# Optimization experiments

Measured on AMD Instinct MI355X. Metric: run time of the kernel, lower is better.

Reference implementation:

```python
import math
import jax, jax.numpy as jnp
import numpy as np

B, T, C = 2, 2048, 1024
H, HKV, HD = 16, 4, 64  # n_head, n_kv_head, head_dim
G = H // HKV            # GQA groups
WS = 1024               # sliding window size
GATE_CH = 32


def setup_inputs() -> dict:
    key = jax.random.key(0)
    ks = jax.random.split(key, 8)
    x = jax.random.normal(ks[0], (B, T, C), dtype=jnp.float32)
    ve = jax.random.normal(ks[1], (B, T, HKV * HD), dtype=jnp.float32)
    # realistic RoPE tables: half head_dim frequencies
    d = HD // 2
    inv_freq = 1.0 / (10000.0 ** (jnp.arange(d, dtype=jnp.float32) / d))
    angles = jnp.arange(T, dtype=jnp.float32)[:, None] * inv_freq[None, :]  # (T, d)
    cos = jnp.cos(angles)[None, :, None, :]  # (1, T, 1, d)
    sin = jnp.sin(angles)[None, :, None, :]
    s = 0.02
    Wq = s * jax.random.normal(ks[2], (C, H * HD), dtype=jnp.float32)
    Wk = s * jax.random.normal(ks[3], (C, HKV * HD), dtype=jnp.float32)
    Wv = s * jax.random.normal(ks[4], (C, HKV * HD), dtype=jnp.float32)
    Wproj = s * jax.random.normal(ks[5], (C, C), dtype=jnp.float32)
    Wg = s * jax.random.normal(ks[6], (GATE_CH, HKV), dtype=jnp.float32)
    return {"x": x, "ve": ve, "cos": cos, "sin": sin,
            "Wq": Wq, "Wk": Wk, "Wv": Wv, "Wproj": Wproj, "Wg": Wg, "ws": WS}


def _rope(u, cos, sin):
    d = u.shape[-1] // 2
    u1, u2 = u[..., :d], u[..., d:]
    return jnp.concatenate([u1 * cos + u2 * sin, -u1 * sin + u2 * cos], axis=-1)


def _rmsnorm(u):
    eps = jnp.finfo(u.dtype).eps
    return u * jax.lax.rsqrt(jnp.mean(u * u, axis=-1, keepdims=True) + eps)


def reference(x, ve, cos, sin, Wq, Wk, Wv, Wproj, Wg, ws):
    b, t, c = x.shape
    q = (x @ Wq).reshape(b, t, H, HD)
    k = (x @ Wk).reshape(b, t, HKV, HD)
    v = (x @ Wv).reshape(b, t, HKV, HD)
    # value-embedding gate: 2*sigmoid over first 32 channels of x
    gate = 2.0 * jax.nn.sigmoid(x[..., :GATE_CH] @ Wg)  # (b, t, HKV)
    v = v + gate[..., None] * ve.reshape(b, t, HKV, HD)
    q = _rmsnorm(_rope(q, cos, sin))
    k = _rmsnorm(_rope(k, cos, sin))
    # GQA: view q as (b, t, HKV, G, HD), contract against shared k/v per kv-head
    qg = q.reshape(b, t, HKV, G, HD)
    scale = 1.0 / math.sqrt(HD)
    scores = jnp.einsum('bqhgd,bkhd->bhgqk', qg, k) * scale  # (b, HKV, G, t, t)
    pos = jnp.arange(t)
    # key j attends iff i - ws + 1 <= j <= i (sliding causal window)
    mask = (pos[None, :] >= pos[:, None] - ws + 1) & (pos[None, :] <= pos[:, None])
    scores = jnp.where(mask[None, None, None], scores, -jnp.inf)
    attn = jax.nn.softmax(scores, axis=-1)
    y = jnp.einsum('bhgqk,bkhd->bqhgd', attn, v).reshape(b, t, H * HD)
    return y @ Wproj
```

## Files before the change

### kernel.cpp

```cpp
#include <hip/hip_runtime.h>
#include <hip/hip_bf16.h>

#define Bq 2
#define Tq 2048
#define Cq 1024
#define Hq 16
#define HKVq 4
#define HDq 64
#define Gq 4
#define WSq 1024
#define GATE_CHq 32

typedef __attribute__((ext_vector_type(8))) short short8;
typedef __attribute__((ext_vector_type(4))) float f32x4;
typedef __attribute__((ext_vector_type(2))) unsigned int u32x2;
typedef unsigned int u32;
typedef unsigned short u16;

#if __has_builtin(__builtin_amdgcn_exp2f)
#define EXP2(x) __builtin_amdgcn_exp2f(x)
#else
#define EXP2(x) exp2f(x)
#endif

__device__ __forceinline__ u16 f2bf(float f) {
  u32 u = __float_as_uint(f);
  u32 r = (u + 0x7FFFu + ((u >> 16) & 1u)) >> 16;
  return (u16)r;
}
__device__ __forceinline__ float bf2f(u16 u) {
  return __uint_as_float(((u32)u) << 16);
}

__device__ __forceinline__ void gl_lds16(const u16* g, u16* l) {
  __builtin_amdgcn_global_load_lds(
      (const u32 __attribute__((address_space(1)))*)g,
      (u32 __attribute__((address_space(3)))*)l, 16, 0, 0);
}

template <bool BF16OUT>
__global__ __launch_bounds__(256) void gemm_bt(
    const u16* __restrict__ A, const u16* __restrict__ Bt,
    void* __restrict__ Cv, int M, int N, int K) {
  __shared__ __attribute__((aligned(16))) u16 As[64 * 32];
  __shared__ __attribute__((aligned(16))) u16 Bs[128 * 32];

  const int bm0 = blockIdx.y * 64, bn0 = blockIdx.x * 128;
  const int tid = threadIdx.x;
  const int w = tid >> 6, lane = tid & 63;
  const int wm = (w >> 1) * 32, wn = (w & 1) * 64;
  const int quad = lane >> 4, l16 = lane & 15;

  f32x4 acc[2][4];
#pragma unroll
  for (int mt = 0; mt < 2; mt++)
#pragma unroll
    for (int nt = 0; nt < 4; nt++) acc[mt][nt] = (f32x4){0.f, 0.f, 0.f, 0.f};

  const int mA = tid >> 2, gpA = tid & 3;
  const int goffA = mA * K + (gpA ^ ((mA >> 1) & 3)) * 8;
  int goffB[2];
#pragma unroll
  for (int i = 0; i < 2; i++) {
    int s = i * 256 + tid;
    int m = s >> 2, gp = s & 3;
    goffB[i] = m * K + (gp ^ ((m >> 1) & 3)) * 8;
  }
  const u16* Ab = A + (long)bm0 * K;
  const u16* Bb = Bt + (long)bn0 * K;

  const u16* pA[2];
  const u16* pB[4];
#pragma unroll
  for (int t = 0; t < 2; t++) {
    int ml = wm + t * 16 + l16;
    pA[t] = &As[(ml * 4 + (quad ^ ((ml >> 1) & 3))) * 8];
  }
#pragma unroll
  for (int t = 0; t < 4; t++) {
    int nl = wn + t * 16 + l16;
    pB[t] = &Bs[(nl * 4 + (quad ^ ((nl >> 1) & 3))) * 8];
  }

  for (int k0 = 0; k0 < K; k0 += 32) {
    __syncthreads();
    gl_lds16(Ab + goffA + k0, &As[(w * 64) * 8]);
#pragma unroll
    for (int i = 0; i < 2; i++)
      gl_lds16(Bb + goffB[i] + k0, &Bs[(i * 256 + w * 64) * 8]);
    __syncthreads();

    short8 af[2], bf[4];
#pragma unroll
    for (int t = 0; t < 2; t++) af[t] = *(const short8*)pA[t];
#pragma unroll
    for (int t = 0; t < 4; t++) bf[t] = *(const short8*)pB[t];
#pragma unroll
    for (int mt = 0; mt < 2; mt++)
#pragma unroll
      for (int nt = 0; nt < 4; nt++)
        acc[mt][nt] = __builtin_amdgcn_mfma_f32_16x16x32_bf16(
            af[mt], bf[nt], acc[mt][nt], 0, 0, 0);
  }

#pragma unroll
  for (int mt = 0; mt < 2; mt++)
#pragma unroll
    for (int nt = 0; nt < 4; nt++) {
      int row0 = bm0 + wm + mt * 16 + quad * 4;
      int col = bn0 + wn + nt * 16 + l16;
#pragma unroll
      for (int r = 0; r < 4; r++) {
        if (BF16OUT)
          ((u16*)Cv)[(long)(row0 + r) * N + col] = f2bf(acc[mt][nt][r]);
        else
          ((float*)Cv)[(long)(row0 + r) * N + col] = acc[mt][nt][r];
      }
    }
}

__global__ __launch_bounds__(256) void cast_bf16(const float* __restrict__ S,
                                                 u16* __restrict__ D) {
  int i = (blockIdx.x * 256 + threadIdx.x) * 8;
  float4 a = *(const float4*)(S + i);
  float4 b = *(const float4*)(S + i + 4);
  union { short8 v; u16 u[8]; } o;
  o.u[0] = f2bf(a.x); o.u[1] = f2bf(a.y); o.u[2] = f2bf(a.z); o.u[3] = f2bf(a.w);
  o.u[4] = f2bf(b.x); o.u[5] = f2bf(b.y); o.u[6] = f2bf(b.z); o.u[7] = f2bf(b.w);
  *(short8*)(D + i) = o.v;
}

__device__ __forceinline__ void wtrans_body(const float* __restrict__ S,
                                            u16* __restrict__ D, int N, int n0,
                                            int k0, float (*tile)[65]) {
  int tid = threadIdx.x;
#pragma unroll
  for (int i = 0; i < 16; i++) {
    int idx = i * 256 + tid;
    int kl = idx >> 6, nl = idx & 63;
    tile[kl][nl] = S[(long)(k0 + kl) * N + n0 + nl];
  }
  __syncthreads();
#pragma unroll
  for (int i = 0; i < 16; i++) {
    int idx = i * 256 + tid;
    int nl = idx >> 6, kl = idx & 63;
    D[(long)(n0 + nl) * 1024 + k0 + kl] = f2bf(tile[kl][nl]);
  }
}

__global__ __launch_bounds__(256) void wtrans(const float* __restrict__ S,
                                              u16* __restrict__ D, int N) {
  __shared__ float tile[64][65];
  wtrans_body(S, D, N, blockIdx.x * 64, blockIdx.y * 64, tile);
}

__global__ __launch_bounds__(256) void wtrans_qkv(
    const float* __restrict__ Wq, const float* __restrict__ Wk,
    const float* __restrict__ Wv, u16* __restrict__ D) {
  __shared__ float tile[64][65];
  int bx = blockIdx.x;
  const float* S;
  u16* Dst;
  int N, nb;
  if (bx < 16)      { S = Wq; N = 1024; nb = bx;      Dst = D; }
  else if (bx < 20) { S = Wk; N = 256;  nb = bx - 16; Dst = D + 1024 * 1024; }
  else              { S = Wv; N = 256;  nb = bx - 20; Dst = D + 1280 * 1024; }
  wtrans_body(S, Dst, N, nb * 64, blockIdx.y * 64, tile);
}

__device__ __forceinline__ float rope_rms(float u, int lane, float c, float s) {
  float up = __shfl_xor(u, 32);
  float r = (lane < 32) ? (u * c + up * s) : (u * c - up * s);
  float sum = r * r;
#pragma unroll
  for (int off = 32; off >= 1; off >>= 1) sum += __shfl_xor(sum, off);
  return r * rsqrtf(sum * (1.f / 64.f) + 1.1920928955078125e-07f);
}

__global__ __launch_bounds__(256) void postproc(
    const float* __restrict__ x, const float* __restrict__ ve,
    const float* __restrict__ cosp, const float* __restrict__ sinp,
    const float* __restrict__ Wg, const u16* __restrict__ QKV,
    u16* __restrict__ Qb, u16* __restrict__ Kb, u16* __restrict__ Vb) {
  int bt = blockIdx.x;
  int b = bt >> 11;
  int t = bt & (Tq - 1);
  int tid = threadIdx.x;
  int w = tid >> 6;
  int lane = tid & 63;
  const u16* row = QKV + (long)bt * 1536;

  float c = cosp[t * 32 + (lane & 31)];
  float s = sinp[t * 32 + (lane & 31)];

  float pg = 0.f;
  if (lane < 32) pg = x[(long)bt * Cq + lane] * Wg[lane * HKVq + w];
#pragma unroll
  for (int off = 16; off >= 1; off >>= 1) pg += __shfl_xor(pg, off);
  float z = __shfl(pg, 0);
  float gate = 2.f / (1.f + expf(-z));

  long vi = (long)bt * (HKVq * HDq) + w * HDq + lane;
  float v = bf2f(row[1280 + w * HDq + lane]) + gate * ve[vi];
  Vb[((long)((b * 4 + w) * Tq + t)) * 64 + lane] = f2bf(v);

  float kv = rope_rms(bf2f(row[1024 + w * HDq + lane]), lane, c, s);
  Kb[((long)((b * 4 + w) * Tq + t)) * 64 + lane] = f2bf(kv);

#pragma unroll
  for (int hi = 0; hi < 4; hi++) {
    int h = hi * 4 + w;
    float q = rope_rms(bf2f(row[h * HDq + lane]), lane, c, s);
    Qb[((long)(((b * 4 + hi) * 4 + w) * Tq + t)) * 64 + lane] = f2bf(q);
  }
}

__global__ __launch_bounds__(256) void vtrans(const u16* __restrict__ Vb,
                                              u16* __restrict__ Vtb) {
  __shared__ u16 tile[64][74];
  int bh = blockIdx.y;
  int t0 = blockIdx.x * 64;
  int tid = threadIdx.x;
  const u16* src = Vb + ((long)bh * Tq + t0) * 64;
  u16* dst = Vtb + (long)bh * 64 * Tq + t0;
#pragma unroll
  for (int i = 0; i < 16; i++) {
    int idx = i * 256 + tid;
    int r = idx >> 6, cl = idx & 63;
    tile[r][cl] = src[(long)r * 64 + cl];
  }
  __syncthreads();
#pragma unroll
  for (int i = 0; i < 16; i++) {
    int idx = i * 256 + tid;
    int d = idx >> 6, t = idx & 63;
    dst[(long)d * Tq + t] = tile[t][d];
  }
}

#define CEXP 0.18033688011112042f
#define CEXP8 1.4426950408889634f

__device__ __forceinline__ void attn_tile(
    int k0, bool maskC, bool maskW, int qpos, int quad, int l16,
    const u16* __restrict__ Ks, const u16* __restrict__ Vts,
    u32* __restrict__ myPs, short8 QB0, short8 QB1, f32x4* O, float& lsum) {
  f32x4 S4[4];
#pragma unroll
  for (int nt = 0; nt < 4; nt++) {
    int key = nt * 16 + l16;
    short8 kb0 = *(const short8*)(&Ks[key * 64 + ((quad ^ (key & 7)) * 8)]);
    short8 kb1 = *(const short8*)(&Ks[key * 64 + (((quad + 4) ^ (key & 7)) * 8)]);
    f32x4 acc = (f32x4){0.f, 0.f, 0.f, 0.f};
    acc = __builtin_amdgcn_mfma_f32_16x16x32_bf16(kb0, QB0, acc, 0, 0, 0);
    acc = __builtin_amdgcn_mfma_f32_16x16x32_bf16(kb1, QB1, acc, 0, 0, 0);
    S4[nt] = acc;
  }

  float Pv[4][4];
#pragma unroll
  for (int nt = 0; nt < 4; nt++) {
#pragma unroll
    for (int r = 0; r < 4; r++) {
      float sv = S4[nt][r];
      if (maskC || maskW) {
        int kpos = k0 + nt * 16 + quad * 4 + r;
        bool valid = true;
        if (maskC) valid = valid && (kpos <= qpos);
        if (maskW) valid = valid && (kpos >= qpos - (WSq - 1));
        sv = valid ? sv : -1e30f;
      }
      float p = EXP2(__builtin_fmaf(sv, CEXP, -CEXP8));
      Pv[nt][r] = p;
      lsum += p;
    }
  }

#pragma unroll
  for (int nt = 0; nt < 4; nt++) {
    u32x2 pk;
#pragma unroll
    for (int rp = 0; rp < 2; rp++) {
      u32 lo = __float_as_uint(Pv[nt][2 * rp]) + 0x8000u;
      u32 hi = __float_as_uint(Pv[nt][2 * rp + 1]) + 0x8000u;
      pk[rp] = __builtin_amdgcn_perm(hi, lo, 0x07060302u);
    }
    *(u32x2*)(&myPs[l16 * 36 + 8 * nt + 2 * quad]) = pk;
  }
  short8 pa0 = *(const short8*)(&myPs[l16 * 36 + quad * 4]);
  short8 pa1 = *(const short8*)(&myPs[l16 * 36 + 16 + quad * 4]);

#pragma unroll
  for (int nt = 0; nt < 4; nt++) {
    int d = nt * 16 + l16;
    short8 vb0 = *(const short8*)(&Vts[d * 64 + ((quad ^ (d & 7)) * 8)]);
    short8 vb1 = *(const short8*)(&Vts[d * 64 + (((quad + 4) ^ (d & 7)) * 8)]);
    O[nt] = __builtin_amdgcn_mfma_f32_16x16x32_bf16(pa0, vb0, O[nt], 0, 0, 0);
    O[nt] = __builtin_amdgcn_mfma_f32_16x16x32_bf16(pa1, vb1, O[nt], 0, 0, 0);
  }
}

__global__ __launch_bounds__(256) void attn_mfma(
    const u16* __restrict__ Qb, const u16* __restrict__ Kb,
    const u16* __restrict__ Vtb, u16* __restrict__ Yb) {
  __shared__ __attribute__((aligned(16))) u16 Ks[64 * 64];
  __shared__ __attribute__((aligned(16))) u16 Vts[64 * 64];
  __shared__ __attribute__((aligned(16))) u32 Ps[4][16 * 36];

  int bid = blockIdx.x;
  int qt = bid & 127;
  int hkv = (bid >> 7) & 3;
  int b = bid >> 9;
  int tid = threadIdx.x;
  int g = tid >> 6;
  int lane = tid & 63;
  int quad = lane >> 4;
  int l16 = lane & 15;
  int qpos = qt * 16 + l16;

  const u16* qb =
      Qb + ((long)(((b * 4 + hkv) * 4 + g) * Tq + qt * 16 + l16)) * 64 + quad * 8;
  short8 QB0 = *(const short8*)(qb);
  short8 QB1 = *(const short8*)(qb + 32);

  f32x4 O[4];
#pragma unroll
  for (int nt = 0; nt < 4; nt++) O[nt] = (f32x4){0.f, 0.f, 0.f, 0.f};
  float lsum = 0.f;

  int lo = qt * 16 - (WSq - 1);
  int st = (lo < 0 ? 0 : lo) >> 6;
  int et = (qt * 16 + 15) >> 6;
  bool needW = (qt >= 64);

  const u16* Kbase = Kb + ((long)((b * 4 + hkv) * Tq)) * 64;
  const u16* Vbase = Vtb + ((long)((b * 4 + hkv) * 64)) * Tq;
  u32* myPs = &Ps[g][0];

  int rowoffK[2], rowoffV[2];
#pragma unroll
  for (int i = 0; i < 2; i++) {
    int s = i * 256 + tid;
    int row = s >> 3, gl = s & 7;
    rowoffK[i] = row * 64 + (gl ^ (row & 7)) * 8;
    rowoffV[i] = row * Tq + (gl ^ (row & 7)) * 8;
  }

  for (int kt = st; kt <= et; kt++) {
    int k0 = kt * 64;
    __syncthreads();
#pragma unroll
    for (int i = 0; i < 2; i++) {
      gl_lds16(Kbase + (long)k0 * 64 + rowoffK[i], &Ks[(i * 256 + g * 64) * 8]);
      gl_lds16(Vbase + k0 + rowoffV[i], &Vts[(i * 256 + g * 64) * 8]);
    }
    __syncthreads();

    if (kt == et)
      attn_tile(k0, true, needW && (kt == st), qpos, quad, l16, Ks, Vts, myPs,
                QB0, QB1, O, lsum);
    else if (kt == st && needW)
      attn_tile(k0, false, true, qpos, quad, l16, Ks, Vts, myPs, QB0, QB1, O,
                lsum);
    else
      attn_tile(k0, false, false, qpos, quad, l16, Ks, Vts, myPs, QB0, QB1, O,
                lsum);
  }

  lsum += __shfl_xor(lsum, 16);
  lsum += __shfl_xor(lsum, 32);
  float invl[4];
#pragma unroll
  for (int r = 0; r < 4; r++) invl[r] = 1.f / __shfl(lsum, quad * 4 + r);

  int h = hkv * 4 + g;
#pragma unroll
  for (int nt = 0; nt < 4; nt++)
#pragma unroll
    for (int r = 0; r < 4; r++)
      Yb[((long)(b * Tq + qt * 16 + quad * 4 + r)) * 1024 + h * 64 + nt * 16 +
         l16] = f2bf(O[nt][r] * invl[r]);
}

extern "C" void kernel_launch(void* const* d_in, const int* in_sizes, int n_in,
                              void* d_out, int out_size, void* d_ws,
                              size_t ws_size, hipStream_t stream) {
  const float* x     = (const float*)d_in[0];
  const float* ve    = (const float*)d_in[1];
  const float* cosp  = (const float*)d_in[2];
  const float* sinp  = (const float*)d_in[3];
  const float* Wq    = (const float*)d_in[4];
  const float* Wk    = (const float*)d_in[5];
  const float* Wv    = (const float*)d_in[6];
  const float* Wproj = (const float*)d_in[7];
  const float* Wg    = (const float*)d_in[8];

  char* base = (char*)d_ws;
  u16* xb     = (u16*)(base);
  u16* Qb     = xb;
  u16* WqkvT  = (u16*)(base + 8388608);
  u16* Kb     = WqkvT;
  u16* WprojT = (u16*)(base + 11534336);
  u16* QKVb   = (u16*)(base + 13631488);
  u16* Vb     = (u16*)(base + 26214400);
  u16* Vtb    = (u16*)(base + 28311552);
  u16* Yb     = (u16*)(base + 30408704);
  float* out = (float*)d_out;

  cast_bf16<<<2048, 256, 0, stream>>>(x, xb);
  wtrans_qkv<<<dim3(24, 16), 256, 0, stream>>>(Wq, Wk, Wv, WqkvT);
  wtrans<<<dim3(16, 16), 256, 0, stream>>>(Wproj, WprojT, 1024);

  gemm_bt<true><<<dim3(12, 64), 256, 0, stream>>>(xb, WqkvT, QKVb, 4096, 1536,
                                                  1024);
  postproc<<<Bq * Tq, 256, 0, stream>>>(x, ve, cosp, sinp, Wg, QKVb, Qb, Kb,
                                        Vb);
  vtrans<<<dim3(32, 8), 256, 0, stream>>>(Vb, Vtb);
  attn_mfma<<<Bq * HKVq * (Tq / 16), 256, 0, stream>>>(Qb, Kb, Vtb, Yb);
  gemm_bt<false><<<dim3(8, 64), 256, 0, stream>>>(Yb, WprojT, out, 4096, 1024,
                                                  1024);
}
```

Measured before the change: 190.5 us.

## Process 32 queries per wave in attention and merge weight transpose kernels

```diff
diff --git a/kernel.cpp b/kernel.cpp
--- a/kernel.cpp
+++ b/kernel.cpp
@@ -149,23 +149,19 @@
   }
 }
 
-__global__ __launch_bounds__(256) void wtrans(const float* __restrict__ S,
-                                              u16* __restrict__ D, int N) {
-  __shared__ float tile[64][65];
-  wtrans_body(S, D, N, blockIdx.x * 64, blockIdx.y * 64, tile);
-}
-
-__global__ __launch_bounds__(256) void wtrans_qkv(
+__global__ __launch_bounds__(256) void wtrans_all(
     const float* __restrict__ Wq, const float* __restrict__ Wk,
-    const float* __restrict__ Wv, u16* __restrict__ D) {
+    const float* __restrict__ Wv, const float* __restrict__ Wproj,
+    u16* __restrict__ Dqkv, u16* __restrict__ Dproj) {
   __shared__ float tile[64][65];
   int bx = blockIdx.x;
   const float* S;
   u16* Dst;
   int N, nb;
-  if (bx < 16)      { S = Wq; N = 1024; nb = bx;      Dst = D; }
-  else if (bx < 20) { S = Wk; N = 256;  nb = bx - 16; Dst = D + 1024 * 1024; }
-  else              { S = Wv; N = 256;  nb = bx - 20; Dst = D + 1280 * 1024; }
+  if (bx < 16)      { S = Wq;    N = 1024; nb = bx;      Dst = Dqkv; }
+  else if (bx < 20) { S = Wk;    N = 256;  nb = bx - 16; Dst = Dqkv + 1024 * 1024; }
+  else if (bx < 24) { S = Wv;    N = 256;  nb = bx - 20; Dst = Dqkv + 1280 * 1024; }
+  else              { S = Wproj; N = 1024; nb = bx - 24; Dst = Dproj; }
   wtrans_body(S, Dst, N, nb * 64, blockIdx.y * 64, tile);
 }
 
@@ -242,97 +238,116 @@
 #define CEXP 0.18033688011112042f
 #define CEXP8 1.4426950408889634f
 
-__device__ __forceinline__ void attn_tile(
-    int k0, bool maskC, bool maskW, int qpos, int quad, int l16,
-    const u16* __restrict__ Ks, const u16* __restrict__ Vts,
-    u32* __restrict__ myPs, short8 QB0, short8 QB1, f32x4* O, float& lsum) {
-  f32x4 S4[4];
-#pragma unroll
-  for (int nt = 0; nt < 4; nt++) {
-    int key = nt * 16 + l16;
+template <bool MASK>
+__device__ __forceinline__ void attn_tile32(
+    int k0, int q0, int quad, int l16, const u16* __restrict__ Ks,
+    const u16* __restrict__ Vts, u32* __restrict__ myPs,
+    const short8 (&QB)[2][2], f32x4 (&O)[2][4], float (&lsum)[2]) {
+  f32x4 S4[4][2];
+#pragma unroll
+  for (int kt4 = 0; kt4 < 4; kt4++) {
+    int key = kt4 * 16 + l16;
     short8 kb0 = *(const short8*)(&Ks[key * 64 + ((quad ^ (key & 7)) * 8)]);
     short8 kb1 = *(const short8*)(&Ks[key * 64 + (((quad + 4) ^ (key & 7)) * 8)]);
-    f32x4 acc = (f32x4){0.f, 0.f, 0.f, 0.f};
-    acc = __builtin_amdgcn_mfma_f32_16x16x32_bf16(kb0, QB0, acc, 0, 0, 0);
-    acc = __builtin_amdgcn_mfma_f32_16x16x32_bf16(kb1, QB1, acc, 0, 0, 0);
-    S4[nt] = acc;
-  }
-
-  float Pv[4][4];
-#pragma unroll
-  for (int nt = 0; nt < 4; nt++) {
-#pragma unroll
-    for (int r = 0; r < 4; r++) {
-      float sv = S4[nt][r];
-      if (maskC || maskW) {
-        int kpos = k0 + nt * 16 + quad * 4 + r;
-        bool valid = true;
-        if (maskC) valid = valid && (kpos <= qpos);
-        if (maskW) valid = valid && (kpos >= qpos - (WSq - 1));
-        sv = valid ? sv : -1e30f;
+#pragma unroll
+    for (int qj = 0; qj < 2; qj++) {
+      f32x4 acc = (f32x4){0.f, 0.f, 0.f, 0.f};
+      acc = __builtin_amdgcn_mfma_f32_16x16x32_bf16(kb0, QB[qj][0], acc, 0, 0, 0);
+      acc = __builtin_amdgcn_mfma_f32_16x16x32_bf16(kb1, QB[qj][1], acc, 0, 0, 0);
+      S4[kt4][qj] = acc;
+    }
+  }
+
+#pragma unroll
+  for (int kt4 = 0; kt4 < 4; kt4++)
+#pragma unroll
+    for (int qj = 0; qj < 2; qj++) {
+      float Pv[4];
+#pragma unroll
+      for (int r = 0; r < 4; r++) {
+        float sv = S4[kt4][qj][r];
+        if (MASK) {
+          int kpos = k0 + kt4 * 16 + quad * 4 + r;
+          int qpos = q0 + qj * 16 + l16;
+          bool valid = (kpos <= qpos) && (kpos >= qpos - (WSq - 1));
+          sv = valid ? sv : -1e30f;
+        }
+        float p = EXP2(__builtin_fmaf(sv, CEXP, -CEXP8));
+        Pv[r] = p;
+        lsum[qj] += p;
       }
-      float p = EXP2(__builtin_fmaf(sv, CEXP, -CEXP8));
-      Pv[nt][r] = p;
-      lsum += p;
+      u32x2 pk;
+#pragma unroll
+      for (int rp = 0; rp < 2; rp++) {
+        u32 lo = __float_as_uint(Pv[2 * rp]) + 0x8000u;
+        u32 hi = __float_as_uint(Pv[2 * rp + 1]) + 0x8000u;
+        pk[rp] = __builtin_amdgcn_perm(hi, lo, 0x07060302u);
+      }
+      *(u32x2*)(&myPs[(qj * 16 + l16) * 36 + kt4 * 8 + quad * 2]) = pk;
     }
-  }
-
-#pragma unroll
-  for (int nt = 0; nt < 4; nt++) {
-    u32x2 pk;
-#pragma unroll
-    for (int rp = 0; rp < 2; rp++) {
-      u32 lo = __float_as_uint(Pv[nt][2 * rp]) + 0x8000u;
-      u32 hi = __float_as_uint(Pv[nt][2 * rp + 1]) + 0x8000u;
-      pk[rp] = __builtin_amdgcn_perm(hi, lo, 0x07060302u);
-    }
-    *(u32x2*)(&myPs[l16 * 36 + 8 * nt + 2 * quad]) = pk;
-  }
-  short8 pa0 = *(const short8*)(&myPs[l16 * 36 + quad * 4]);
-  short8 pa1 = *(const short8*)(&myPs[l16 * 36 + 16 + quad * 4]);
-
+
+  short8 vb[4][2];
 #pragma unroll
   for (int nt = 0; nt < 4; nt++) {
     int d = nt * 16 + l16;
-    short8 vb0 = *(const short8*)(&Vts[d * 64 + ((quad ^ (d & 7)) * 8)]);
-    short8 vb1 = *(const short8*)(&Vts[d * 64 + (((quad + 4) ^ (d & 7)) * 8)]);
-    O[nt] = __builtin_amdgcn_mfma_f32_16x16x32_bf16(pa0, vb0, O[nt], 0, 0, 0);
-    O[nt] = __builtin_amdgcn_mfma_f32_16x16x32_bf16(pa1, vb1, O[nt], 0, 0, 0);
-  }
-}
-
-__global__ __launch_bounds__(256) void attn_mfma(
+    vb[nt][0] = *(const short8*)(&Vts[d * 64 + ((quad ^ (d & 7)) * 8)]);
+    vb[nt][1] = *(const short8*)(&Vts[d * 64 + (((quad + 4) ^ (d & 7)) * 8)]);
+  }
+
+#pragma unroll
+  for (int qj = 0; qj < 2; qj++) {
+    const u32* prow = &myPs[(qj * 16 + l16) * 36];
+    short8 pa0 = *(const short8*)(prow + quad * 4);
+    short8 pa1 = *(const short8*)(prow + 16 + quad * 4);
+#pragma unroll
+    for (int nt = 0; nt < 4; nt++) {
+      O[qj][nt] =
+          __builtin_amdgcn_mfma_f32_16x16x32_bf16(pa0, vb[nt][0], O[qj][nt], 0, 0, 0);
+      O[qj][nt] =
+          __builtin_amdgcn_mfma_f32_16x16x32_bf16(pa1, vb[nt][1], O[qj][nt], 0, 0, 0);
+    }
+  }
+}
+
+__global__ __launch_bounds__(256, 2) void attn_mfma(
     const u16* __restrict__ Qb, const u16* __restrict__ Kb,
     const u16* __restrict__ Vtb, u16* __restrict__ Yb) {
   __shared__ __attribute__((aligned(16))) u16 Ks[64 * 64];
   __shared__ __attribute__((aligned(16))) u16 Vts[64 * 64];
-  __shared__ __attribute__((aligned(16))) u32 Ps[4][16 * 36];
+  __shared__ __attribute__((aligned(16))) u32 Ps[4][32 * 36];
 
   int bid = blockIdx.x;
-  int qt = bid & 127;
-  int hkv = (bid >> 7) & 3;
-  int b = bid >> 9;
+  int bh = bid & 7;
+  int qt32 = bid >> 3;
+  int hkv = bh & 3;
+  int b = bh >> 2;
+  int q0 = qt32 * 32;
   int tid = threadIdx.x;
   int g = tid >> 6;
   int lane = tid & 63;
   int quad = lane >> 4;
   int l16 = lane & 15;
-  int qpos = qt * 16 + l16;
-
-  const u16* qb =
-      Qb + ((long)(((b * 4 + hkv) * 4 + g) * Tq + qt * 16 + l16)) * 64 + quad * 8;
-  short8 QB0 = *(const short8*)(qb);
-  short8 QB1 = *(const short8*)(qb + 32);
-
-  f32x4 O[4];
-#pragma unroll
-  for (int nt = 0; nt < 4; nt++) O[nt] = (f32x4){0.f, 0.f, 0.f, 0.f};
-  float lsum = 0.f;
-
-  int lo = qt * 16 - (WSq - 1);
+
+  short8 QB[2][2];
+#pragma unroll
+  for (int qj = 0; qj < 2; qj++) {
+    const u16* qb = Qb +
+        ((long)(((b * 4 + hkv) * 4 + g) * Tq + q0 + qj * 16 + l16)) * 64 +
+        quad * 8;
+    QB[qj][0] = *(const short8*)(qb);
+    QB[qj][1] = *(const short8*)(qb + 32);
+  }
+
+  f32x4 O[2][4];
+#pragma unroll
+  for (int qj = 0; qj < 2; qj++)
+#pragma unroll
+    for (int nt = 0; nt < 4; nt++) O[qj][nt] = (f32x4){0.f, 0.f, 0.f, 0.f};
+  float lsum[2] = {0.f, 0.f};
+
+  int lo = q0 - (WSq - 1);
   int st = (lo < 0 ? 0 : lo) >> 6;
-  int et = (qt * 16 + 15) >> 6;
-  bool needW = (qt >= 64);
+  int et = (q0 + 31) >> 6;
 
   const u16* Kbase = Kb + ((long)((b * 4 + hkv) * Tq)) * 64;
   const u16* Vbase = Vtb + ((long)((b * 4 + hkv) * 64)) * Tq;
@@ -357,30 +372,33 @@
     }
     __syncthreads();
 
-    if (kt == et)
-      attn_tile(k0, true, needW && (kt == st), qpos, quad, l16, Ks, Vts, myPs,
-                QB0, QB1, O, lsum);
-    else if (kt == st && needW)
-      attn_tile(k0, false, true, qpos, quad, l16, Ks, Vts, myPs, QB0, QB1, O,
-                lsum);
+    bool needC = (k0 > q0 - 63);
+    bool needW = (k0 < q0 - 992);
+    if (needC || needW)
+      attn_tile32<true>(k0, q0, quad, l16, Ks, Vts, myPs, QB, O, lsum);
     else
-      attn_tile(k0, false, false, qpos, quad, l16, Ks, Vts, myPs, QB0, QB1, O,
-                lsum);
-  }
-
-  lsum += __shfl_xor(lsum, 16);
-  lsum += __shfl_xor(lsum, 32);
-  float invl[4];
-#pragma unroll
-  for (int r = 0; r < 4; r++) invl[r] = 1.f / __shfl(lsum, quad * 4 + r);
+      attn_tile32<false>(k0, q0, quad, l16, Ks, Vts, myPs, QB, O, lsum);
+  }
+
+#pragma unroll
+  for (int qj = 0; qj < 2; qj++) {
+    lsum[qj] += __shfl_xor(lsum[qj], 16);
+    lsum[qj] += __shfl_xor(lsum[qj], 32);
+  }
 
   int h = hkv * 4 + g;
 #pragma unroll
-  for (int nt = 0; nt < 4; nt++)
-#pragma unroll
-    for (int r = 0; r < 4; r++)
-      Yb[((long)(b * Tq + qt * 16 + quad * 4 + r)) * 1024 + h * 64 + nt * 16 +
-         l16] = f2bf(O[nt][r] * invl[r]);
+  for (int qj = 0; qj < 2; qj++) {
+    float invl[4];
+#pragma unroll
+    for (int r = 0; r < 4; r++) invl[r] = 1.f / __shfl(lsum[qj], quad * 4 + r);
+#pragma unroll
+    for (int nt = 0; nt < 4; nt++)
+#pragma unroll
+      for (int r = 0; r < 4; r++)
+        Yb[((long)(b * Tq + q0 + qj * 16 + quad * 4 + r)) * 1024 + h * 64 +
+           nt * 16 + l16] = f2bf(O[qj][nt][r] * invl[r]);
+  }
 }
 
 extern "C" void kernel_launch(void* const* d_in, const int* in_sizes, int n_in,
@@ -409,15 +427,14 @@
   float* out = (float*)d_out;
 
   cast_bf16<<<2048, 256, 0, stream>>>(x, xb);
-  wtrans_qkv<<<dim3(24, 16), 256, 0, stream>>>(Wq, Wk, Wv, WqkvT);
-  wtrans<<<dim3(16, 16), 256, 0, stream>>>(Wproj, WprojT, 1024);
-
+  wtrans_all<<<dim3(40, 16), 256, 0, stream>>>(Wq, Wk, Wv, Wproj, WqkvT,
+                                               WprojT);
   gemm_bt<true><<<dim3(12, 64), 256, 0, stream>>>(xb, WqkvT, QKVb, 4096, 1536,
                                                   1024);
   postproc<<<Bq * Tq, 256, 0, stream>>>(x, ve, cosp, sinp, Wg, QKVb, Qb, Kb,
                                         Vb);
   vtrans<<<dim3(32, 8), 256, 0, stream>>>(Vb, Vtb);
-  attn_mfma<<<Bq * HKVq * (Tq / 16), 256, 0, stream>>>(Qb, Kb, Vtb, Yb);
+  attn_mfma<<<512, 256, 0, stream>>>(Qb, Kb, Vtb, Yb);
   gemm_bt<false><<<dim3(8, 64), 256, 0, stream>>>(Yb, WprojT, out, 4096, 1024,
                                                   1024);
 }
```

Result: faster. 186.2 us (-2.2%).
